# Kernel optimization log

Hardware: AMD Instinct MI355X
Metric: run time of the kernel (lower is better)

## Reference

```python
import jax, jax.numpy as jnp
import numpy as np
from jax import lax

B, S, D, T = 64, 256, 1024, 60
HIST = 20  # last-20 window of attn / decoder-state history


def setup_inputs() -> dict:
    key = jax.random.key(0)
    ks = jax.random.split(key, 8)
    e_outputs = jax.random.normal(ks[0], (B, S, D), jnp.float32)
    queries = jax.random.normal(ks[1], (B, T, D), jnp.float32)
    # attention weights over source frames: rows sum to 1
    attns = jax.nn.softmax(jax.random.normal(ks[2], (B, T, S), jnp.float32), axis=-1)
    g = 0.02
    Wr = jax.random.normal(ks[3], (D, 1), jnp.float32) * g
    br = jnp.zeros((1,), jnp.float32)
    Wa = jax.random.normal(ks[4], (D, 1), jnp.float32) * g
    ba = jnp.zeros((1,), jnp.float32)
    Wq = jax.random.normal(ks[5], (D, D), jnp.float32) / np.sqrt(D)
    Wn = jax.random.normal(ks[6], (2 * D, 1), jnp.float32) * g
    bn = jnp.zeros((1,), jnp.float32)
    return {"e_outputs": e_outputs, "queries": queries, "attns": attns,
            "Wr": Wr, "br": br, "Wa": Wa, "ba": ba, "Wq": Wq, "Wn": Wn, "bn": bn}


def reference(e_outputs, queries, attns, Wr, br, Wa, ba, Wq, Wn, bn):
    Bn, Sn, Dn = e_outputs.shape
    # decay1[i] = (i+1)/20 ; decay2[i] = 1-(i+1)/50, zero-padded past 50 frames
    decay1 = (jnp.arange(HIST, dtype=jnp.float32) + 1.0) / 20.0
    idx = jnp.arange(Sn, dtype=jnp.float32)
    add0 = jnp.where(idx < 50, 1.0 - (idx + 1.0) / 50.0, 0.0)
    add_state0 = add0[None, :, None]                       # [1,S,1]
    mem0 = e_outputs * add_state0                          # [B,S,D]
    abuf0 = jnp.zeros((HIST, Bn, Sn), e_outputs.dtype)
    qbuf0 = jnp.zeros((HIST, Bn, Dn), e_outputs.dtype)

    def step(carry, x):
        mem, add_state, abuf, qbuf, i = carry
        attn_i, q_i = x                                    # [B,S], [B,D]
        # read: selected frame before memory update
        sel = jnp.einsum('bs,bsd->bd', attn_i, mem)
        # roll history buffers (newest at slot HIST-1)
        abuf = jnp.concatenate([abuf[1:], attn_i[None]], axis=0)
        qbuf = jnp.concatenate([qbuf[1:], q_i[None]], axis=0)
        k = jnp.minimum(i + 1, HIST)
        valid = jnp.arange(HIST) >= (HIST - k)
        temp = jax.nn.softmax(jnp.where(valid, decay1, -jnp.inf))
        attn_w = jnp.einsum('t,tbs->bs', temp, abuf)       # decayed attn sum
        query_s = jnp.einsum('t,tbd->bd', temp, qbuf)      # decayed query sum
        remove_prob = jax.nn.sigmoid(q_i @ Wr + br)[:, :, None]   # [B,1,1]
        add_prob = jax.nn.sigmoid(q_i @ Wa + ba)[:, :, None]      # [B,1,1]
        sim = jax.nn.sigmoid(jnp.einsum('bsd,bd->bs', mem, query_s @ Wq))[..., None]
        mem = mem * (1.0 - remove_prob * attn_w[..., None] * sim)
        last_ctx = jnp.einsum('bs,bsd->bd', attn_w, e_outputs)[:, None, :]
        cat = jnp.concatenate([e_outputs, jnp.broadcast_to(last_ctx, e_outputs.shape)], axis=-1)
        nxt = jax.nn.sigmoid(cat @ Wn + bn)                # [B,S,1]
        mem = mem + e_outputs * (1.0 - add_state) * (add_prob * nxt)
        add_state = add_state + (1.0 - add_state) * (add_prob * nxt)
        return (mem, add_state, abuf, qbuf, i + 1), sel

    init = (mem0, jnp.broadcast_to(add_state0, (Bn, Sn, 1)), abuf0, qbuf0, jnp.int32(0))
    xs = (attns.transpose(1, 0, 2), queries.transpose(1, 0, 2))
    _, sels = lax.scan(step, init, xs)
    return sels.transpose(1, 0, 2)                         # [B,T,D]
```

## Files before the change

kernel.cpp:

```cpp
#include <hip/hip_runtime.h>
#include <math.h>


#define Bn 64
#define Sn 256
#define Dn 1024
#define Tn 60
#define HISTn 20
#define LDK 72

typedef __bf16 bf16x8 __attribute__((ext_vector_type(8)));
typedef float f32x4 __attribute__((ext_vector_type(4)));
typedef unsigned short us8 __attribute__((ext_vector_type(8)));

__device__ __forceinline__ float bf2f(unsigned short u){
  unsigned int x = ((unsigned int)u) << 16; float f; __builtin_memcpy(&f,&x,4); return f;
}
__device__ __forceinline__ unsigned short f2bf(float f){
  unsigned int x; __builtin_memcpy(&x,&f,4);
  unsigned int lsb = (x >> 16) & 1u;
  x += 0x7fffu + lsb;
  return (unsigned short)(x >> 16);
}
__device__ __forceinline__ float sigmoidf_(float x){ return 1.0f/(1.0f+expf(-x)); }

__global__ __launch_bounds__(256) void conv_qw(
    const float* __restrict__ Q, const float* __restrict__ Wr,
    const float* __restrict__ br, const float* __restrict__ Wa,
    const float* __restrict__ ba, const float* __restrict__ Wq,
    float* __restrict__ rp, float* __restrict__ ap,
    unsigned short* __restrict__ Qbf, unsigned short* __restrict__ WT)
{
  int tid = threadIdx.x;
  if (blockIdx.x < Bn*Tn){
    int row = blockIdx.x;
    float4 x = ((const float4*)(Q + (size_t)row*Dn))[tid];
    float4 a = ((const float4*)Wr)[tid];
    float4 b = ((const float4*)Wa)[tid];
    unsigned short o[4] = {f2bf(x.x), f2bf(x.y), f2bf(x.z), f2bf(x.w)};
    *(uint2*)&Qbf[(size_t)row*Dn + tid*4] = *(uint2*)o;
    float s1 = x.x*a.x + x.y*a.y + x.z*a.z + x.w*a.w;
    float s2 = x.x*b.x + x.y*b.y + x.z*b.z + x.w*b.w;
    for (int off = 32; off; off >>= 1){
      s1 += __shfl_down(s1, off, 64);
      s2 += __shfl_down(s2, off, 64);
    }
    __shared__ float r1[4], r2[4];
    int lane = tid & 63, wv = tid >> 6;
    if (lane == 0){ r1[wv] = s1; r2[wv] = s2; }
    __syncthreads();
    if (tid == 0){
      rp[row] = sigmoidf_(r1[0]+r1[1]+r1[2]+r1[3] + br[0]);
      ap[row] = sigmoidf_(r2[0]+r2[1]+r2[2]+r2[3] + ba[0]);
    }
  } else {
    __shared__ __align__(16) unsigned short Tt[64][LDK];
    int t = blockIdx.x - Bn*Tn;
    int n0 = (t >> 4)*64, k0 = (t & 15)*64;
    int kl = tid >> 4, nl4 = (tid & 15)*4;
    #pragma unroll
    for (int it = 0; it < 4; it++){
      int k = kl + it*16;
      float4 v = *(const float4*)&Wq[(size_t)(k0+k)*Dn + n0 + nl4];
      Tt[nl4+0][k] = f2bf(v.x); Tt[nl4+1][k] = f2bf(v.y);
      Tt[nl4+2][k] = f2bf(v.z); Tt[nl4+3][k] = f2bf(v.w);
    }
    __syncthreads();
    int nr = tid >> 2, kg = (tid & 3)*16;
    *(us8*)&WT[(size_t)(n0+nr)*Dn + k0+kg]   = *(us8*)&Tt[nr][kg];
    *(us8*)&WT[(size_t)(n0+nr)*Dn + k0+kg+8] = *(us8*)&Tt[nr][kg+8];
  }
}

__global__ __launch_bounds__(256) void conv_e(
    const float* __restrict__ E, unsigned short* __restrict__ Ebf)
{
  size_t i = (size_t)blockIdx.x*256 + threadIdx.x;
  float4 v = ((const float4*)E)[i];
  unsigned short o[4] = {f2bf(v.x), f2bf(v.y), f2bf(v.z), f2bf(v.w)};
  ((uint2*)Ebf)[i] = *(uint2*)o;
}

__global__ __launch_bounds__(256) void gemm_qw(
    const unsigned short* __restrict__ Qbf,
    const unsigned short* __restrict__ WT,
    unsigned short* __restrict__ QWbf)
{
  __shared__ __align__(16) unsigned short As[64][LDK], Bs[64][LDK];
  int m0 = blockIdx.x*64, n0 = blockIdx.y*64;
  int tid = threadIdx.x, lane = tid & 63, wave = tid >> 6;
  int quad = lane >> 4, l16 = lane & 15;
  f32x4 acc[4];
  #pragma unroll
  for (int nt=0;nt<4;nt++)
    #pragma unroll
    for (int r=0;r<4;r++) acc[nt][r]=0.f;
  int sr = tid >> 2, sk = (tid & 3)*16;
  for (int k0 = 0; k0 < Dn; k0 += 64){
    *(us8*)&As[sr][sk]   = *(const us8*)&Qbf[(size_t)(m0+sr)*Dn + k0+sk];
    *(us8*)&As[sr][sk+8] = *(const us8*)&Qbf[(size_t)(m0+sr)*Dn + k0+sk+8];
    *(us8*)&Bs[sr][sk]   = *(const us8*)&WT[(size_t)(n0+sr)*Dn + k0+sk];
    *(us8*)&Bs[sr][sk+8] = *(const us8*)&WT[(size_t)(n0+sr)*Dn + k0+sk+8];
    __syncthreads();
    #pragma unroll
    for (int kk = 0; kk < 64; kk += 32){
      bf16x8 a = *(const bf16x8*)&As[wave*16 + l16][kk + quad*8];
      #pragma unroll
      for (int nt=0;nt<4;nt++){
        bf16x8 bb = *(const bf16x8*)&Bs[nt*16 + l16][kk + quad*8];
        acc[nt] = __builtin_amdgcn_mfma_f32_16x16x32_bf16(a, bb, acc[nt], 0, 0, 0);
      }
    }
    __syncthreads();
  }
  #pragma unroll
  for (int nt=0;nt<4;nt++)
    #pragma unroll
    for (int r=0;r<4;r++){
      int m = m0 + wave*16 + quad*4 + r;
      int n = n0 + nt*16 + l16;
      QWbf[(size_t)m*Dn + n] = f2bf(acc[nt][r]);
    }
}

__global__ __launch_bounds__(256) void gemm_g(
    const unsigned short* __restrict__ QWbf,
    const unsigned short* __restrict__ Ebf,
    const float* __restrict__ Wn,
    float* __restrict__ G, float* __restrict__ eW1, float* __restrict__ eW2)
{
  __shared__ __align__(16) unsigned short As[64][LDK], Bs[32][LDK];
  int b = blockIdx.x, n0 = blockIdx.y*32;
  int tid = threadIdx.x, lane = tid & 63, wave = tid >> 6;
  int quad = lane >> 4, l16 = lane & 15;
  f32x4 acc[2];
  #pragma unroll
  for (int nt=0;nt<2;nt++)
    #pragma unroll
    for (int r=0;r<4;r++) acc[nt][r]=0.f;
  int sr = tid >> 2, sk = (tid & 3)*16;
  int brw = tid >> 3, bk = (tid & 7)*8;
  float d1 = 0.f, d2 = 0.f;
  for (int k0 = 0; k0 < Dn; k0 += 64){
    if (sr < Tn){
      *(us8*)&As[sr][sk]   = *(const us8*)&QWbf[((size_t)(b*Tn + sr))*Dn + k0+sk];
      *(us8*)&As[sr][sk+8] = *(const us8*)&QWbf[((size_t)(b*Tn + sr))*Dn + k0+sk+8];
    } else {
      us8 z = (us8)0;
      *(us8*)&As[sr][sk] = z; *(us8*)&As[sr][sk+8] = z;
    }
    us8 ev = *(const us8*)&Ebf[((size_t)(b*Sn + n0 + brw))*Dn + k0 + bk];
    *(us8*)&Bs[brw][bk] = ev;
    float4 w10 = *(const float4*)&Wn[k0 + bk];
    float4 w11 = *(const float4*)&Wn[k0 + bk + 4];
    float4 w20 = *(const float4*)&Wn[Dn + k0 + bk];
    float4 w21 = *(const float4*)&Wn[Dn + k0 + bk + 4];
    float e0 = bf2f(ev[0]), e1 = bf2f(ev[1]), e2 = bf2f(ev[2]), e3 = bf2f(ev[3]);
    float e4 = bf2f(ev[4]), e5 = bf2f(ev[5]), e6 = bf2f(ev[6]), e7 = bf2f(ev[7]);
    d1 += e0*w10.x + e1*w10.y + e2*w10.z + e3*w10.w
        + e4*w11.x + e5*w11.y + e6*w11.z + e7*w11.w;
    d2 += e0*w20.x + e1*w20.y + e2*w20.z + e3*w20.w
        + e4*w21.x + e5*w21.y + e6*w21.z + e7*w21.w;
    __syncthreads();
    #pragma unroll
    for (int kk = 0; kk < 64; kk += 32){
      bf16x8 a = *(const bf16x8*)&As[wave*16 + l16][kk + quad*8];
      #pragma unroll
      for (int nt=0;nt<2;nt++){
        bf16x8 bb = *(const bf16x8*)&Bs[nt*16 + l16][kk + quad*8];
        acc[nt] = __builtin_amdgcn_mfma_f32_16x16x32_bf16(a, bb, acc[nt], 0, 0, 0);
      }
    }
    __syncthreads();
  }
  d1 += __shfl_down(d1, 4, 64); d1 += __shfl_down(d1, 2, 64); d1 += __shfl_down(d1, 1, 64);
  d2 += __shfl_down(d2, 4, 64); d2 += __shfl_down(d2, 2, 64); d2 += __shfl_down(d2, 1, 64);
  if ((tid & 7) == 0){
    eW1[b*Sn + n0 + brw] = d1;
    eW2[b*Sn + n0 + brw] = d2;
  }
  #pragma unroll
  for (int nt=0;nt<2;nt++)
    #pragma unroll
    for (int r=0;r<4;r++){
      int t = wave*16 + quad*4 + r;
      int s = n0 + nt*16 + l16;
      if (t < Tn) G[((size_t)(b*Tn + t))*Sn + s] = acc[nt][r];
    }
}

__global__ __launch_bounds__(256) void scan_m(
    const float* __restrict__ At,
    const float* __restrict__ G,
    const float* __restrict__ rp,
    const float* __restrict__ ap,
    const float* __restrict__ eW1,
    const float* __restrict__ eW2,
    const float* __restrict__ bnp,
    unsigned short* __restrict__ Pbf)
{
  int b = blockIdx.x, tid = threadIdx.x;
  int lane = tid & 63, wv = tid >> 6;
  __shared__ float Rsh[Tn], lcs[Tn];
  float4 e2v = ((const float4*)(eW2 + (size_t)b*Sn))[lane];
  const float* at_base = At + (size_t)b*Tn*Sn;
  #pragma unroll
  for (int w = 0; w < 15; w++){
    int j = wv + w*4;
    float4 a4 = ((const float4*)(at_base + (size_t)j*Sn))[lane];
    float v = a4.x*e2v.x + a4.y*e2v.y + a4.z*e2v.z + a4.w*e2v.w;
    #pragma unroll
    for (int off = 32; off; off >>= 1) v += __shfl_down(v, off, 64);
    if (lane == 0) Rsh[j] = v;
  }
  __syncthreads();
  if (tid < Tn){
    int i = tid;
    int j0 = (i - HISTn + 1 > 0) ? i - HISTn + 1 : 0;
    float num = 0.f, den = 0.f;
    for (int j = j0; j <= i; j++){
      float wj = expf(0.05f*(j+1));
      num += wj * Rsh[j];
      den += wj;
    }
    lcs[i] = num / den;
  }
  __syncthreads();
  int s = tid;
  float M = (s < 50) ? (1.0f - (s+1)/50.0f) : 0.0f;
  float A = M;
  float bnv = bnp[0];
  float e1 = eW1[b*Sn + s];
  const float* at_b = At + (size_t)b*Tn*Sn + s;
  const float* G_b  = G  + (size_t)b*Tn*Sn + s;
  unsigned short* P_b = Pbf + (size_t)b*Tn*Sn + s;
  const float* rp_b = rp + b*Tn;
  const float* ap_b = ap + b*Tn;
  float num_a = 0.f, num_q = 0.f, den = 0.f;
  #pragma unroll
  for (int i = 0; i < Tn; i++){
    float wi = expf(0.05f*(i+1));
    float a_new = at_b[i*Sn];
    float g_new = G_b[i*Sn];
    num_a += wi * a_new;
    num_q += wi * g_new;
    den   += wi;
    if (i >= HISTn){
      float wo = expf(0.05f*(i-HISTn+1));
      num_a -= wo * at_b[(i-HISTn)*Sn];
      num_q -= wo * G_b[(i-HISTn)*Sn];
      den   -= wo;
    }
    float inv = 1.0f / den;
    float aw = num_a * inv;
    float qd = num_q * inv;
    P_b[i*Sn] = f2bf(a_new * M);
    float sim = sigmoidf_(M * qd);
    float nxt = sigmoidf_(e1 + lcs[i] + bnv);
    M = M * (1.0f - rp_b[i] * aw * sim);
    float g = (1.0f - A) * ap_b[i] * nxt;
    M += g; A += g;
  }
}

__global__ __launch_bounds__(256) void gemm_sels(
    const unsigned short* __restrict__ Pbf,
    const unsigned short* __restrict__ Ebf,
    float* __restrict__ out)
{
  __shared__ __align__(16) unsigned short As[64][LDK], Bs[64][LDK];
  int b = blockIdx.x, n0 = blockIdx.y*64;
  int tid = threadIdx.x, lane = tid & 63, wave = tid >> 6;
  int quad = lane >> 4, l16 = lane & 15;
  f32x4 acc[4];
  #pragma unroll
  for (int nt=0;nt<4;nt++)
    #pragma unroll
    for (int r=0;r<4;r++) acc[nt][r]=0.f;
  int sr = tid >> 2, sk = (tid & 3)*16;
  for (int k0 = 0; k0 < Sn; k0 += 64){
    if (sr < Tn){
      *(us8*)&As[sr][sk]   = *(const us8*)&Pbf[((size_t)(b*Tn + sr))*Sn + k0+sk];
      *(us8*)&As[sr][sk+8] = *(const us8*)&Pbf[((size_t)(b*Tn + sr))*Sn + k0+sk+8];
    } else {
      us8 z = (us8)0;
      *(us8*)&As[sr][sk] = z; *(us8*)&As[sr][sk+8] = z;
    }
    {
      const unsigned short* ep = &Ebf[((size_t)(b*Sn + k0 + sr))*Dn + n0 + sk];
      us8 e0 = *(const us8*)ep;
      us8 e1 = *(const us8*)(ep + 8);
      #pragma unroll
      for (int j=0;j<8;j++){
        Bs[sk+j][sr]   = e0[j];
        Bs[sk+8+j][sr] = e1[j];
      }
    }
    __syncthreads();
    #pragma unroll
    for (int kk = 0; kk < 64; kk += 32){
      bf16x8 a = *(const bf16x8*)&As[wave*16 + l16][kk + quad*8];
      #pragma unroll
      for (int nt=0;nt<4;nt++){
        bf16x8 bb = *(const bf16x8*)&Bs[nt*16 + l16][kk + quad*8];
        acc[nt] = __builtin_amdgcn_mfma_f32_16x16x32_bf16(a, bb, acc[nt], 0, 0, 0);
      }
    }
    __syncthreads();
  }
  #pragma unroll
  for (int nt=0;nt<4;nt++)
    #pragma unroll
    for (int r=0;r<4;r++){
      int t = wave*16 + quad*4 + r;
      int d = n0 + nt*16 + l16;
      if (t < Tn) out[((size_t)(b*Tn + t))*Dn + d] = acc[nt][r];
    }
}

extern "C" void kernel_launch(void* const* d_in, const int* in_sizes, int n_in,
                              void* d_out, int out_size, void* d_ws, size_t ws_size,
                              hipStream_t stream)
{
  const float* E  = (const float*)d_in[0];
  const float* Q  = (const float*)d_in[1];
  const float* At = (const float*)d_in[2];
  const float* Wr = (const float*)d_in[3];
  const float* br = (const float*)d_in[4];
  const float* Wa = (const float*)d_in[5];
  const float* ba = (const float*)d_in[6];
  const float* Wq = (const float*)d_in[7];
  const float* Wn = (const float*)d_in[8];
  const float* bnp= (const float*)d_in[9];

  char* ws = (char*)d_ws;
  float* rp  = (float*)ws; ws += (size_t)Bn*Tn*4;
  float* ap  = (float*)ws; ws += (size_t)Bn*Tn*4;
  float* eW1 = (float*)ws; ws += (size_t)Bn*Sn*4;
  float* eW2 = (float*)ws; ws += (size_t)Bn*Sn*4;
  unsigned short* Qbf  = (unsigned short*)ws; ws += (size_t)Bn*Tn*Dn*2;
  unsigned short* WT   = (unsigned short*)ws; ws += (size_t)Dn*Dn*2;
  unsigned short* QWbf = (unsigned short*)ws; ws += (size_t)Bn*Tn*Dn*2;
  unsigned short* Ebf  = (unsigned short*)ws; ws += (size_t)Bn*Sn*Dn*2;
  float* G = (float*)ws; ws += (size_t)Bn*Tn*Sn*4;
  unsigned short* Pbf = (unsigned short*)ws; ws += (size_t)Bn*Tn*Sn*2;

  conv_qw<<<Bn*Tn + 256, 256, 0, stream>>>(Q, Wr, br, Wa, ba, Wq, rp, ap, Qbf, WT);
  conv_e<<<(Bn*Sn*Dn/4)/256, 256, 0, stream>>>(E, Ebf);
  gemm_qw<<<dim3(Bn*Tn/64, Dn/64), 256, 0, stream>>>(Qbf, WT, QWbf);
  gemm_g<<<dim3(Bn, Sn/32), 256, 0, stream>>>(QWbf, Ebf, Wn, G, eW1, eW2);
  scan_m<<<Bn, 256, 0, stream>>>(At, G, rp, ap, eW1, eW2, bnp, Pbf);
  gemm_sels<<<dim3(Bn, Dn/64), 256, 0, stream>>>(Pbf, Ebf, (float*)d_out);
}
```

Baseline: 212.8 us.

## Split scan across more blocks, move Wn dots into conversion, precompute decay weights

The per-batch scan kernel is split in two: a small kernel computes the decayed last-context terms, and the recurrence now runs on 64-thread blocks over 64-column slices of S, which gives four times as many blocks and stages the At and G slices in shared memory. The e·Wn dot products move from the bf16 GEMM into the fp32 conversion kernel, which is now one wave per row. The expf calls for the decay weights are replaced by running multiplications with a constant. This adds one kernel launch and changes the numerics slightly, since the Wn dots now use fp32 inputs instead of bf16.

```diff
diff --git a/kernel.cpp b/kernel.cpp
--- a/kernel.cpp
+++ b/kernel.cpp
@@ -8,14 +8,13 @@
 #define Tn 60
 #define HISTn 20
 #define LDK 72
+#define K05 1.0512710963760241f
+#define EINV 0.36787944117144233f
 
 typedef __bf16 bf16x8 __attribute__((ext_vector_type(8)));
 typedef float f32x4 __attribute__((ext_vector_type(4)));
 typedef unsigned short us8 __attribute__((ext_vector_type(8)));
 
-__device__ __forceinline__ float bf2f(unsigned short u){
-  unsigned int x = ((unsigned int)u) << 16; float f; __builtin_memcpy(&f,&x,4); return f;
-}
 __device__ __forceinline__ unsigned short f2bf(float f){
   unsigned int x; __builtin_memcpy(&x,&f,4);
   unsigned int lsb = (x >> 16) & 1u;
@@ -72,13 +71,32 @@
   }
 }
 
-__global__ __launch_bounds__(256) void conv_e(
-    const float* __restrict__ E, unsigned short* __restrict__ Ebf)
-{
-  size_t i = (size_t)blockIdx.x*256 + threadIdx.x;
-  float4 v = ((const float4*)E)[i];
-  unsigned short o[4] = {f2bf(v.x), f2bf(v.y), f2bf(v.z), f2bf(v.w)};
-  ((uint2*)Ebf)[i] = *(uint2*)o;
+__global__ __launch_bounds__(64) void conv_e(
+    const float* __restrict__ E, const float* __restrict__ Wn,
+    unsigned short* __restrict__ Ebf,
+    float* __restrict__ eW1, float* __restrict__ eW2)
+{
+  int row = blockIdx.x, t = threadIdx.x;
+  const float* er = E + (size_t)row*Dn;
+  unsigned short* ebr = Ebf + (size_t)row*Dn;
+  float d1 = 0.f, d2 = 0.f;
+  #pragma unroll
+  for (int c = 0; c < 4; c++){
+    int idx = c*64 + t;
+    float4 v = ((const float4*)er)[idx];
+    float4 w1 = ((const float4*)Wn)[idx];
+    float4 w2 = ((const float4*)(Wn + Dn))[idx];
+    unsigned short o[4] = {f2bf(v.x), f2bf(v.y), f2bf(v.z), f2bf(v.w)};
+    ((uint2*)ebr)[idx] = *(uint2*)o;
+    d1 += v.x*w1.x + v.y*w1.y + v.z*w1.z + v.w*w1.w;
+    d2 += v.x*w2.x + v.y*w2.y + v.z*w2.z + v.w*w2.w;
+  }
+  #pragma unroll
+  for (int off = 32; off; off >>= 1){
+    d1 += __shfl_down(d1, off, 64);
+    d2 += __shfl_down(d2, off, 64);
+  }
+  if (t == 0){ eW1[row] = d1; eW2[row] = d2; }
 }
 
 __global__ __launch_bounds__(256) void gemm_qw(
@@ -126,8 +144,7 @@
 __global__ __launch_bounds__(256) void gemm_g(
     const unsigned short* __restrict__ QWbf,
     const unsigned short* __restrict__ Ebf,
-    const float* __restrict__ Wn,
-    float* __restrict__ G, float* __restrict__ eW1, float* __restrict__ eW2)
+    float* __restrict__ G)
 {
   __shared__ __align__(16) unsigned short As[64][LDK], Bs[32][LDK];
   int b = blockIdx.x, n0 = blockIdx.y*32;
@@ -140,7 +157,6 @@
     for (int r=0;r<4;r++) acc[nt][r]=0.f;
   int sr = tid >> 2, sk = (tid & 3)*16;
   int brw = tid >> 3, bk = (tid & 7)*8;
-  float d1 = 0.f, d2 = 0.f;
   for (int k0 = 0; k0 < Dn; k0 += 64){
     if (sr < Tn){
       *(us8*)&As[sr][sk]   = *(const us8*)&QWbf[((size_t)(b*Tn + sr))*Dn + k0+sk];
@@ -149,18 +165,7 @@
       us8 z = (us8)0;
       *(us8*)&As[sr][sk] = z; *(us8*)&As[sr][sk+8] = z;
     }
-    us8 ev = *(const us8*)&Ebf[((size_t)(b*Sn + n0 + brw))*Dn + k0 + bk];
-    *(us8*)&Bs[brw][bk] = ev;
-    float4 w10 = *(const float4*)&Wn[k0 + bk];
-    float4 w11 = *(const float4*)&Wn[k0 + bk + 4];
-    float4 w20 = *(const float4*)&Wn[Dn + k0 + bk];
-    float4 w21 = *(const float4*)&Wn[Dn + k0 + bk + 4];
-    float e0 = bf2f(ev[0]), e1 = bf2f(ev[1]), e2 = bf2f(ev[2]), e3 = bf2f(ev[3]);
-    float e4 = bf2f(ev[4]), e5 = bf2f(ev[5]), e6 = bf2f(ev[6]), e7 = bf2f(ev[7]);
-    d1 += e0*w10.x + e1*w10.y + e2*w10.z + e3*w10.w
-        + e4*w11.x + e5*w11.y + e6*w11.z + e7*w11.w;
-    d2 += e0*w20.x + e1*w20.y + e2*w20.z + e3*w20.w
-        + e4*w21.x + e5*w21.y + e6*w21.z + e7*w21.w;
+    *(us8*)&Bs[brw][bk] = *(const us8*)&Ebf[((size_t)(b*Sn + n0 + brw))*Dn + k0 + bk];
     __syncthreads();
     #pragma unroll
     for (int kk = 0; kk < 64; kk += 32){
@@ -173,12 +178,6 @@
     }
     __syncthreads();
   }
-  d1 += __shfl_down(d1, 4, 64); d1 += __shfl_down(d1, 2, 64); d1 += __shfl_down(d1, 1, 64);
-  d2 += __shfl_down(d2, 4, 64); d2 += __shfl_down(d2, 2, 64); d2 += __shfl_down(d2, 1, 64);
-  if ((tid & 7) == 0){
-    eW1[b*Sn + n0 + brw] = d1;
-    eW2[b*Sn + n0 + brw] = d2;
-  }
   #pragma unroll
   for (int nt=0;nt<2;nt++)
     #pragma unroll
@@ -189,76 +188,98 @@
     }
 }
 
-__global__ __launch_bounds__(256) void scan_m(
+__global__ __launch_bounds__(256) void kR_lc(
+    const float* __restrict__ At,
+    const float* __restrict__ eW2,
+    float* __restrict__ lc)
+{
+  int b = blockIdx.x, tid = threadIdx.x;
+  int lane = tid & 63, wv = tid >> 6;
+  __shared__ float Rsh[Tn];
+  float4 e2v = ((const float4*)(eW2 + (size_t)b*Sn))[lane];
+  const float* at_b = At + (size_t)b*Tn*Sn;
+  #pragma unroll
+  for (int w = 0; w < 15; w++){
+    int j = wv + w*4;
+    float4 a4 = ((const float4*)(at_b + (size_t)j*Sn))[lane];
+    float v = a4.x*e2v.x + a4.y*e2v.y + a4.z*e2v.z + a4.w*e2v.w;
+    #pragma unroll
+    for (int off = 32; off; off >>= 1) v += __shfl_down(v, off, 64);
+    if (lane == 0) Rsh[j] = v;
+  }
+  __syncthreads();
+  if (tid < Tn){
+    int i = tid;
+    int j0 = (i - HISTn + 1 > 0) ? i - HISTn + 1 : 0;
+    float num = 0.f, den = 0.f;
+    float wj = 1.f;
+    for (int j = 0; j <= i; j++){
+      wj *= K05;
+      if (j >= j0){ num += wj * Rsh[j]; den += wj; }
+    }
+    lc[b*Tn + i] = num / den;
+  }
+}
+
+__global__ __launch_bounds__(64) void scan_m(
     const float* __restrict__ At,
     const float* __restrict__ G,
     const float* __restrict__ rp,
     const float* __restrict__ ap,
     const float* __restrict__ eW1,
-    const float* __restrict__ eW2,
+    const float* __restrict__ lc,
     const float* __restrict__ bnp,
     unsigned short* __restrict__ Pbf)
 {
-  int b = blockIdx.x, tid = threadIdx.x;
-  int lane = tid & 63, wv = tid >> 6;
-  __shared__ float Rsh[Tn], lcs[Tn];
-  float4 e2v = ((const float4*)(eW2 + (size_t)b*Sn))[lane];
-  const float* at_base = At + (size_t)b*Tn*Sn;
-  #pragma unroll
-  for (int w = 0; w < 15; w++){
-    int j = wv + w*4;
-    float4 a4 = ((const float4*)(at_base + (size_t)j*Sn))[lane];
-    float v = a4.x*e2v.x + a4.y*e2v.y + a4.z*e2v.z + a4.w*e2v.w;
-    #pragma unroll
-    for (int off = 32; off; off >>= 1) v += __shfl_down(v, off, 64);
-    if (lane == 0) Rsh[j] = v;
+  int b = blockIdx.x, s0 = blockIdx.y * 64;
+  int t = threadIdx.x;
+  __shared__ __align__(16) float AtL[Tn][64], GL[Tn][64];
+  __shared__ float lcs[Tn], rps[Tn], aps[Tn];
+  const float* at_b = At + (size_t)b*Tn*Sn + s0;
+  const float* g_b  = G  + (size_t)b*Tn*Sn + s0;
+  #pragma unroll
+  for (int r0 = 0; r0 < Tn; r0 += 4){
+    int r = r0 + (t >> 4), c4 = (t & 15)*4;
+    float4 av = *(const float4*)&at_b[(size_t)r*Sn + c4];
+    float4 gv = *(const float4*)&g_b[(size_t)r*Sn + c4];
+    *(float4*)&AtL[r][c4] = av;
+    *(float4*)&GL[r][c4]  = gv;
+  }
+  if (t < Tn){
+    lcs[t] = lc[b*Tn + t];
+    rps[t] = rp[b*Tn + t];
+    aps[t] = ap[b*Tn + t];
   }
   __syncthreads();
-  if (tid < Tn){
-    int i = tid;
-    int j0 = (i - HISTn + 1 > 0) ? i - HISTn + 1 : 0;
-    float num = 0.f, den = 0.f;
-    for (int j = j0; j <= i; j++){
-      float wj = expf(0.05f*(j+1));
-      num += wj * Rsh[j];
-      den += wj;
-    }
-    lcs[i] = num / den;
-  }
-  __syncthreads();
-  int s = tid;
+  int s = s0 + t;
   float M = (s < 50) ? (1.0f - (s+1)/50.0f) : 0.0f;
   float A = M;
   float bnv = bnp[0];
   float e1 = eW1[b*Sn + s];
-  const float* at_b = At + (size_t)b*Tn*Sn + s;
-  const float* G_b  = G  + (size_t)b*Tn*Sn + s;
   unsigned short* P_b = Pbf + (size_t)b*Tn*Sn + s;
-  const float* rp_b = rp + b*Tn;
-  const float* ap_b = ap + b*Tn;
-  float num_a = 0.f, num_q = 0.f, den = 0.f;
+  float num_a = 0.f, num_q = 0.f, den = 0.f, wi = 1.f;
   #pragma unroll
   for (int i = 0; i < Tn; i++){
-    float wi = expf(0.05f*(i+1));
-    float a_new = at_b[i*Sn];
-    float g_new = G_b[i*Sn];
+    wi *= K05;
+    float a_new = AtL[i][t];
+    float g_new = GL[i][t];
     num_a += wi * a_new;
     num_q += wi * g_new;
     den   += wi;
     if (i >= HISTn){
-      float wo = expf(0.05f*(i-HISTn+1));
-      num_a -= wo * at_b[(i-HISTn)*Sn];
-      num_q -= wo * G_b[(i-HISTn)*Sn];
+      float wo = wi * EINV;
+      num_a -= wo * AtL[i-HISTn][t];
+      num_q -= wo * GL[i-HISTn][t];
       den   -= wo;
     }
     float inv = 1.0f / den;
     float aw = num_a * inv;
     float qd = num_q * inv;
-    P_b[i*Sn] = f2bf(a_new * M);
+    P_b[(size_t)i*Sn] = f2bf(a_new * M);
     float sim = sigmoidf_(M * qd);
     float nxt = sigmoidf_(e1 + lcs[i] + bnv);
-    M = M * (1.0f - rp_b[i] * aw * sim);
-    float g = (1.0f - A) * ap_b[i] * nxt;
+    M = M * (1.0f - rps[i] * aw * sim);
+    float g = (1.0f - A) * aps[i] * nxt;
     M += g; A += g;
   }
 }
@@ -338,6 +359,7 @@
   float* ap  = (float*)ws; ws += (size_t)Bn*Tn*4;
   float* eW1 = (float*)ws; ws += (size_t)Bn*Sn*4;
   float* eW2 = (float*)ws; ws += (size_t)Bn*Sn*4;
+  float* lcb = (float*)ws; ws += (size_t)Bn*Tn*4;
   unsigned short* Qbf  = (unsigned short*)ws; ws += (size_t)Bn*Tn*Dn*2;
   unsigned short* WT   = (unsigned short*)ws; ws += (size_t)Dn*Dn*2;
   unsigned short* QWbf = (unsigned short*)ws; ws += (size_t)Bn*Tn*Dn*2;
@@ -346,9 +368,10 @@
   unsigned short* Pbf = (unsigned short*)ws; ws += (size_t)Bn*Tn*Sn*2;
 
   conv_qw<<<Bn*Tn + 256, 256, 0, stream>>>(Q, Wr, br, Wa, ba, Wq, rp, ap, Qbf, WT);
-  conv_e<<<(Bn*Sn*Dn/4)/256, 256, 0, stream>>>(E, Ebf);
+  conv_e<<<Bn*Sn, 64, 0, stream>>>(E, Wn, Ebf, eW1, eW2);
   gemm_qw<<<dim3(Bn*Tn/64, Dn/64), 256, 0, stream>>>(Qbf, WT, QWbf);
-  gemm_g<<<dim3(Bn, Sn/32), 256, 0, stream>>>(QWbf, Ebf, Wn, G, eW1, eW2);
-  scan_m<<<Bn, 256, 0, stream>>>(At, G, rp, ap, eW1, eW2, bnp, Pbf);
+  gemm_g<<<dim3(Bn, Sn/32), 256, 0, stream>>>(QWbf, Ebf, G);
+  kR_lc<<<Bn, 256, 0, stream>>>(At, eW2, lcb);
+  scan_m<<<dim3(Bn, Sn/64), 64, 0, stream>>>(At, G, rp, ap, eW1, lcb, bnp, Pbf);
   gemm_sels<<<dim3(Bn, Dn/64), 256, 0, stream>>>(Pbf, Ebf, (float*)d_out);
 }
```

After: 210.0 us. Within noise of the previous version (-1.3%).
